# Kernel tuning notes

Measured on AMD Instinct MI355X. Metric: run time of the kernel, lower is better.

## Reference

```python
import math
import jax, jax.numpy as jnp
import numpy as np

B, NQ, NK, DIM, H, HD = 2, 1024, 2048, 1024, 16, 64


def setup_inputs() -> dict:
    key = jax.random.key(0)
    ks = jax.random.split(key, 12)
    s = 1.0 / math.sqrt(DIM)
    return {
        "q": jax.random.normal(ks[0], (B, NQ, DIM), jnp.float32),
        "k": jax.random.normal(ks[1], (B, NK, DIM), jnp.float32),
        "v": jax.random.normal(ks[2], (B, NK, DIM), jnp.float32),
        "distances": jax.random.uniform(ks[3], (B, NQ, NK), jnp.float32),
        "attn_mask": jax.random.bernoulli(ks[4], 0.5, (B, NQ, NK)),
        "key_padding_mask_q": jax.random.bernoulli(ks[5], 0.5, (B, NQ)),
        "key_padding_mask_k": jax.random.bernoulli(ks[6], 0.5, (B, NK)),
        "Wq": jax.random.normal(ks[7], (H * HD, DIM), jnp.float32) * s,
        "Wk": jax.random.normal(ks[8], (H * HD, DIM), jnp.float32) * s,
        "Wv": jax.random.normal(ks[9], (H * HD, DIM), jnp.float32) * s,
        "Wo": jax.random.normal(ks[10], (DIM, H * HD), jnp.float32) * s,
        "gate_alpha": jnp.float32(0.1),
    }


def reference(q, k, v, distances, attn_mask, key_padding_mask_q,
              key_padding_mask_k, Wq, Wk, Wv, Wo, gate_alpha):
    bsz, q_len, _ = q.shape
    k_len = k.shape[1]
    neg = jnp.finfo(q.dtype).min

    # projections -> (B, H, N, HD)
    qp = (q @ Wq.T).reshape(bsz, q_len, H, HD).transpose(0, 2, 1, 3)
    kp = (k @ Wk.T).reshape(bsz, k_len, H, HD).transpose(0, 2, 1, 3)
    vp = (v @ Wv.T).reshape(bsz, k_len, H, HD).transpose(0, 2, 1, 3)

    scores = jnp.einsum('bhqd,bhkd->bhqk', qp, kp) / math.sqrt(HD)
    scores = jnp.where(attn_mask[:, None, :, :], scores, neg)
    scores = jnp.where(key_padding_mask_k[:, None, None, :], scores, neg)

    attn = jax.nn.softmax(scores, axis=-1)  # (B,H,NQ,NK)

    # distance gating: mask, batch-mean normalize, exponential gate
    d = distances * attn_mask.astype(distances.dtype)
    d = d * key_padding_mask_k[:, None, :].astype(d.dtype)
    mean = d.sum(axis=(-1, -2)) / (q_len * k_len + 1e-6)
    mean = jnp.maximum(mean, 1e-6)[:, None, None]
    d = d / mean
    alpha = jax.nn.softplus(gate_alpha)
    gate = jnp.exp(-alpha * d)[:, None, :, :]  # (B,1,NQ,NK)

    w = attn * gate
    w = w / (w.sum(axis=-1, keepdims=True) + 1e-6)

    out = jnp.einsum('bhqk,bhkd->bhqd', w, vp)
    out = out.transpose(0, 2, 1, 3).reshape(bsz, q_len, H * HD)
    out = out * key_padding_mask_q[:, :, None].astype(out.dtype)
    return out @ Wo.T
```

## Files before the change

### kernel.cpp

```cpp
#include <hip/hip_runtime.h>
#include <hip/hip_bf16.h>
#include <cfloat>

#define B_   2
#define NQ_  1024
#define NK_  2048
#define H_   16
#define HD_  64
#define VPAD 2176
#define GPAD 2112

typedef float  floatx4 __attribute__((ext_vector_type(4)));
typedef __bf16 bf16x8  __attribute__((ext_vector_type(8)));
typedef __bf16 bf16x4  __attribute__((ext_vector_type(4)));

static __device__ __forceinline__ floatx4 mfma16(bf16x8 a, bf16x8 b, floatx4 c) {
    return __builtin_amdgcn_mfma_f32_16x16x32_bf16(a, b, c, 0, 0, 0);
}

struct CvtArgs {
    const float* src[7];
    __bf16*      dst[7];
};

__global__ __launch_bounds__(256) void cvt_kernel(CvtArgs a)
{
    size_t r = (size_t)blockIdx.x * 256 + threadIdx.x;
    int s;
    if (r < 262144)                  { s = 0; }
    else if ((r -= 262144) < 524288) { s = 1; }
    else if ((r -= 524288) < 524288) { s = 2; }
    else { r -= 524288; s = 3 + (int)(r >> 17); r &= 131071; }
    const float* sp = a.src[s] + r * 8;
    float4 f0 = *(const float4*)sp;
    float4 f1 = *(const float4*)(sp + 4);
    bf16x8 o;
    o[0] = (__bf16)f0.x; o[1] = (__bf16)f0.y; o[2] = (__bf16)f0.z; o[3] = (__bf16)f0.w;
    o[4] = (__bf16)f1.x; o[5] = (__bf16)f1.y; o[6] = (__bf16)f1.z; o[7] = (__bf16)f1.w;
    *(bf16x8*)(a.dst[s] + r * 8) = o;
}

__global__ __launch_bounds__(256) void mean_kernel(
    const float* __restrict__ dist, const int* __restrict__ amask,
    const int* __restrict__ kpmk, float* __restrict__ msum)
{
    const int b = blockIdx.y;
    const float* d  = dist  + (size_t)b * NQ_ * NK_;
    const int*   am = amask + (size_t)b * NQ_ * NK_;
    const int*   km = kpmk  + b * NK_;
    const int total = NQ_ * NK_ / 4;
    float s = 0.f;
    for (int i = blockIdx.x * blockDim.x + threadIdx.x; i < total;
         i += gridDim.x * blockDim.x) {
        const int idx = i * 4;
        const int kk  = idx & (NK_ - 1);
        float4 dv = *(const float4*)(d + idx);
        int4   mv = *(const int4*)(am + idx);
        int4   kv = *(const int4*)(km + kk);
        s += (mv.x && kv.x) ? dv.x : 0.f;
        s += (mv.y && kv.y) ? dv.y : 0.f;
        s += (mv.z && kv.z) ? dv.z : 0.f;
        s += (mv.w && kv.w) ? dv.w : 0.f;
    }
    #pragma unroll
    for (int off = 32; off >= 1; off >>= 1) s += __shfl_down(s, off);
    __shared__ float wsum[4];
    if ((threadIdx.x & 63) == 0) wsum[threadIdx.x >> 6] = s;
    __syncthreads();
    if (threadIdx.x == 0)
        atomicAdd(&msum[b], wsum[0] + wsum[1] + wsum[2] + wsum[3]);
}

__global__ __launch_bounds__(256) void gate_kernel(
    const float* __restrict__ dist, const int* __restrict__ amask,
    const int* __restrict__ kpmk, const float* __restrict__ msum,
    const float* __restrict__ galpha, __bf16* __restrict__ gate)
{
    const int b = blockIdx.y;
    const float mean  = fmaxf(msum[b] / ((float)(NQ_ * NK_) + 1e-6f), 1e-6f);
    const float alpha = log1pf(__expf(galpha[0]));
    const float c     = -alpha / mean;
    const int i  = blockIdx.x * 256 + threadIdx.x;
    const int q  = i >> 9;
    const int k4 = (i & 511) * 4;
    const size_t src = ((size_t)b * NQ_ + q) * NK_ + k4;
    float4 dv = *(const float4*)(dist + src);
    int4   mv = *(const int4*)(amask + src);
    int4   kv = *(const int4*)(kpmk + b * NK_ + k4);
    bf16x4 r;
    r[0] = (mv.x && kv.x) ? (__bf16)__expf(c * dv.x) : (__bf16)0.f;
    r[1] = (mv.y && kv.y) ? (__bf16)__expf(c * dv.y) : (__bf16)0.f;
    r[2] = (mv.z && kv.z) ? (__bf16)__expf(c * dv.z) : (__bf16)0.f;
    r[3] = (mv.w && kv.w) ? (__bf16)__expf(c * dv.w) : (__bf16)0.f;
    *(bf16x4*)&gate[((size_t)b * NQ_ + q) * GPAD + k4] = r;
}

template <int MODE>
__global__ __launch_bounds__(256) void gemm64(
    const __bf16* __restrict__ A, const __bf16* __restrict__ Bw,
    void* __restrict__ Cout)
{
    __shared__ __bf16 As[4 * 64 * 8];
    __shared__ __bf16 Bs[4 * 128 * 8];
    const int t    = threadIdx.x;
    const int m0   = blockIdx.x * 64, n0 = blockIdx.y * 128;
    const int w    = t >> 6, lane = t & 63;
    const int lrow = lane & 15, quad = lane >> 4;

    const int rowA = t >> 2, cA = t & 3;
    const int rowB1 = 64 + (t >> 2);
    const __bf16* Ag  = A  + (size_t)(m0 + rowA) * 1024 + cA * 8;
    const __bf16* Bg0 = Bw + (size_t)(n0 + rowA) * 1024 + cA * 8;
    const __bf16* Bg1 = Bw + (size_t)(n0 + rowB1) * 1024 + cA * 8;
    __bf16* AsW  = &As[cA * 512  + rowA * 8];
    __bf16* BsW0 = &Bs[cA * 1024 + rowA * 8];
    __bf16* BsW1 = &Bs[cA * 1024 + rowB1 * 8];

    floatx4 acc[4][2];
    #pragma unroll
    for (int mi = 0; mi < 4; mi++)
        #pragma unroll
        for (int ni = 0; ni < 2; ni++) acc[mi][ni] = floatx4{0.f, 0.f, 0.f, 0.f};

    bf16x8 ar  = *(const bf16x8*)Ag;
    bf16x8 br0 = *(const bf16x8*)Bg0;
    bf16x8 br1 = *(const bf16x8*)Bg1;

    for (int k0 = 0; k0 < 1024; k0 += 32) {
        __syncthreads();
        *(bf16x8*)AsW  = ar;
        *(bf16x8*)BsW0 = br0;
        *(bf16x8*)BsW1 = br1;
        __syncthreads();
        if (k0 + 32 < 1024) {
            ar  = *(const bf16x8*)(Ag  + k0 + 32);
            br0 = *(const bf16x8*)(Bg0 + k0 + 32);
            br1 = *(const bf16x8*)(Bg1 + k0 + 32);
        }
        bf16x8 af[4], bfr[2];
        #pragma unroll
        for (int mi = 0; mi < 4; mi++)
            af[mi] = *(const bf16x8*)&As[quad * 512 + (mi * 16 + lrow) * 8];
        #pragma unroll
        for (int ni = 0; ni < 2; ni++)
            bfr[ni] = *(const bf16x8*)&Bs[quad * 1024 + (w * 32 + ni * 16 + lrow) * 8];
        #pragma unroll
        for (int mi = 0; mi < 4; mi++)
            #pragma unroll
            for (int ni = 0; ni < 2; ni++)
                acc[mi][ni] = mfma16(af[mi], bfr[ni], acc[mi][ni]);
    }

    #pragma unroll
    for (int mi = 0; mi < 4; mi++) {
        #pragma unroll
        for (int ni = 0; ni < 2; ni++) {
            #pragma unroll
            for (int r = 0; r < 4; r++) {
                const float val = acc[mi][ni][r];
                const int m = m0 + mi * 16 + quad * 4 + r;
                const int n = n0 + w * 32 + ni * 16 + lrow;
                if constexpr (MODE == 0) {
                    const int b = m >> 10, q = m & 1023;
                    const int h = n >> 6,  d = n & 63;
                    ((__bf16*)Cout)[(((size_t)(b * 16 + h) * NQ_ + q) << 6) + d] =
                        (__bf16)val;
                } else if constexpr (MODE == 1) {
                    const int b = m >> 11, key = m & 2047;
                    const int h = n >> 6,  d = n & 63;
                    ((__bf16*)Cout)[(((size_t)(b * 16 + h) * NK_ + key) << 6) + d] =
                        (__bf16)val;
                } else if constexpr (MODE == 2) {
                    const int b = m >> 11, key = m & 2047;
                    const int h = n >> 6,  d = n & 63;
                    ((__bf16*)Cout)[((size_t)(b * 16 + h) * HD_ + d) * VPAD + key] =
                        (__bf16)val;
                } else {
                    ((float*)Cout)[(size_t)m * 1024 + n] = val;
                }
            }
        }
    }
}

__global__ __launch_bounds__(256, 2) void attn_kernel(
    const __bf16* __restrict__ qp, const __bf16* __restrict__ kp,
    const __bf16* __restrict__ vpT, const __bf16* __restrict__ gate,
    float* __restrict__ Opart, float* __restrict__ Gpart)
{
    __shared__ __bf16 Ks[64 * 72];
    __shared__ __bf16 Vt[64 * 72];
    __shared__ __bf16 Ps[4][32 * 72];
    const int t    = threadIdx.x;
    const int w    = t >> 6, lane = t & 63;
    const int lrow = lane & 15, quad = lane >> 4;
    const int qt   = blockIdx.x;
    const int bh   = blockIdx.y;
    const int sp   = blockIdx.z;
    const int b    = bh >> 4;
    const int q0   = qt * 128 + w * 32;
    const int k0   = sp * (NK_ / 2);

    bf16x8 qf[2][2];
    #pragma unroll
    for (int qg = 0; qg < 2; qg++) {
        const __bf16* qb = qp + ((size_t)bh * NQ_ + q0 + qg * 16 + lrow) * HD_ +
                           quad * 8;
        qf[qg][0] = *(const bf16x8*)qb;
        qf[qg][1] = *(const bf16x8*)(qb + 32);
    }

    const int srow0 = t >> 3,        sc0 = t & 7;
    const int srow1 = 32 + (t >> 3), sc1 = t & 7;
    const __bf16* Kg = kp  + (size_t)bh * NK_ * HD_;
    const __bf16* Vg = vpT + (size_t)bh * HD_ * VPAD;
    __bf16* KsW0 = &Ks[srow0 * 72 + sc0 * 8];
    __bf16* KsW1 = &Ks[srow1 * 72 + sc1 * 8];
    __bf16* VtW0 = &Vt[srow0 * 72 + sc0 * 8];
    __bf16* VtW1 = &Vt[srow1 * 72 + sc1 * 8];

    const __bf16* grow[2];
    #pragma unroll
    for (int qg = 0; qg < 2; qg++)
        grow[qg] = gate + ((size_t)b * NQ_ + q0 + qg * 16 + lrow) * GPAD;

    float G[2] = {0.f, 0.f};
    floatx4 O[2][4];
    #pragma unroll
    for (int qg = 0; qg < 2; qg++)
        #pragma unroll
        for (int nb = 0; nb < 4; nb++) O[qg][nb] = floatx4{0.f, 0.f, 0.f, 0.f};

    bf16x8 kr0, kr1, vr0, vr1;
    bf16x4 gr[2][4];
    auto loadt = [&](int kb) {
        kr0 = *(const bf16x8*)(Kg + (size_t)(kb + srow0) * HD_ + sc0 * 8);
        kr1 = *(const bf16x8*)(Kg + (size_t)(kb + srow1) * HD_ + sc1 * 8);
        vr0 = *(const bf16x8*)(Vg + (size_t)srow0 * VPAD + kb + sc0 * 8);
        vr1 = *(const bf16x8*)(Vg + (size_t)srow1 * VPAD + kb + sc1 * 8);
        #pragma unroll
        for (int qg = 0; qg < 2; qg++)
            #pragma unroll
            for (int c = 0; c < 4; c++)
                gr[qg][c] = *(const bf16x4*)(grow[qg] + kb + c * 16 + quad * 4);
    };
    loadt(k0);

    for (int kb = k0; kb < k0 + NK_ / 2; kb += 64) {
        __syncthreads();
        *(bf16x8*)KsW0 = kr0;
        *(bf16x8*)KsW1 = kr1;
        *(bf16x8*)VtW0 = vr0;
        *(bf16x8*)VtW1 = vr1;
        __syncthreads();

        bf16x4 gcur[2][4];
        #pragma unroll
        for (int qg = 0; qg < 2; qg++)
            #pragma unroll
            for (int c = 0; c < 4; c++) gcur[qg][c] = gr[qg][c];
        if (kb + 64 < k0 + NK_ / 2) loadt(kb + 64);

        bf16x8 kf0[4], kf1[4];
        #pragma unroll
        for (int c = 0; c < 4; c++) {
            kf0[c] = *(const bf16x8*)&Ks[(c * 16 + lrow) * 72 + quad * 8];
            kf1[c] = *(const bf16x8*)&Ks[(c * 16 + lrow) * 72 + 32 + quad * 8];
        }
        floatx4 s4[2][4];
        #pragma unroll
        for (int qg = 0; qg < 2; qg++)
            #pragma unroll
            for (int c = 0; c < 4; c++) {
                floatx4 a = floatx4{0.f, 0.f, 0.f, 0.f};
                a = mfma16(kf0[c], qf[qg][0], a);
                a = mfma16(kf1[c], qf[qg][1], a);
                s4[qg][c] = a;
            }

        #pragma unroll
        for (int qg = 0; qg < 2; qg++) {
            #pragma unroll
            for (int c = 0; c < 4; c++) {
                const float e0 = __expf(s4[qg][c][0] * 0.125f) * (float)gcur[qg][c][0];
                const float e1 = __expf(s4[qg][c][1] * 0.125f) * (float)gcur[qg][c][1];
                const float e2 = __expf(s4[qg][c][2] * 0.125f) * (float)gcur[qg][c][2];
                const float e3 = __expf(s4[qg][c][3] * 0.125f) * (float)gcur[qg][c][3];
                G[qg] += (e0 + e1) + (e2 + e3);
                bf16x4 pk;
                pk[0] = (__bf16)e0; pk[1] = (__bf16)e1;
                pk[2] = (__bf16)e2; pk[3] = (__bf16)e3;
                *(bf16x4*)&Ps[w][(qg * 16 + lrow) * 72 + c * 16 + quad * 4] = pk;
            }
        }

        bf16x8 pf[2][2];
        #pragma unroll
        for (int qg = 0; qg < 2; qg++)
            #pragma unroll
            for (int tt = 0; tt < 2; tt++)
                pf[qg][tt] = *(const bf16x8*)
                    &Ps[w][(qg * 16 + lrow) * 72 + tt * 32 + quad * 8];
        #pragma unroll
        for (int tt = 0; tt < 2; tt++)
            #pragma unroll
            for (int nb = 0; nb < 4; nb++) {
                bf16x8 vf = *(const bf16x8*)
                    &Vt[(nb * 16 + lrow) * 72 + tt * 32 + quad * 8];
                #pragma unroll
                for (int qg = 0; qg < 2; qg++)
                    O[qg][nb] = mfma16(pf[qg][tt], vf, O[qg][nb]);
            }
    }

    #pragma unroll
    for (int qg = 0; qg < 2; qg++) {
        G[qg] += __shfl_xor(G[qg], 16);
        G[qg] += __shfl_xor(G[qg], 32);
    }
    float* Ob = Opart + ((size_t)(sp * 32 + bh) * NQ_ + q0) * HD_;
    #pragma unroll
    for (int qg = 0; qg < 2; qg++)
        #pragma unroll
        for (int nb = 0; nb < 4; nb++)
            #pragma unroll
            for (int r = 0; r < 4; r++)
                Ob[(size_t)(qg * 16 + quad * 4 + r) * HD_ + nb * 16 + lrow] =
                    O[qg][nb][r];
    if (quad == 0) {
        #pragma unroll
        for (int qg = 0; qg < 2; qg++)
            Gpart[(size_t)(sp * 32 + bh) * NQ_ + q0 + qg * 16 + lrow] = G[qg];
    }
}

__global__ __launch_bounds__(256) void combine_kernel(
    const float* __restrict__ Opart, const float* __restrict__ Gpart,
    const int* __restrict__ kpmq, __bf16* __restrict__ attnout)
{
    const int t  = blockIdx.x * 256 + threadIdx.x;
    const int d4 = (t & 15) * 4;
    const int q  = (t >> 4) & 1023;
    const int bh = t >> 14;
    const int b  = bh >> 4, h = bh & 15;
    const size_t i0 = ((size_t)bh * NQ_ + q) * HD_ + d4;
    const size_t i1 = ((size_t)(32 + bh) * NQ_ + q) * HD_ + d4;
    float4 o0 = *(const float4*)(Opart + i0);
    float4 o1 = *(const float4*)(Opart + i1);
    const float g = Gpart[bh * NQ_ + q] + Gpart[(32 + bh) * NQ_ + q];
    const float f = kpmq[b * NQ_ + q] ? 1.f / (g + 1e-30f) : 0.f;
    bf16x4 r;
    r[0] = (__bf16)((o0.x + o1.x) * f);
    r[1] = (__bf16)((o0.y + o1.y) * f);
    r[2] = (__bf16)((o0.z + o1.z) * f);
    r[3] = (__bf16)((o0.w + o1.w) * f);
    *(bf16x4*)&attnout[((size_t)b * NQ_ + q) * 1024 + h * HD_ + d4] = r;
}

extern "C" void kernel_launch(void* const* d_in, const int* in_sizes, int n_in,
                              void* d_out, int out_size, void* d_ws,
                              size_t ws_size, hipStream_t stream)
{
    const float* q      = (const float*)d_in[0];
    const float* k      = (const float*)d_in[1];
    const float* v      = (const float*)d_in[2];
    const float* dist   = (const float*)d_in[3];
    const int*   amask  = (const int*)d_in[4];
    const int*   kpmq   = (const int*)d_in[5];
    const int*   kpmk   = (const int*)d_in[6];
    const float* Wq     = (const float*)d_in[7];
    const float* Wk     = (const float*)d_in[8];
    const float* Wv     = (const float*)d_in[9];
    const float* Wo     = (const float*)d_in[10];
    const float* galpha = (const float*)d_in[11];

    char* p = (char*)d_ws;
    float*  msum = (float*)p;                 p += 256;
    __bf16* qb   = (__bf16*)p;                p += (size_t)2097152 * 2;
    __bf16* kb   = (__bf16*)p;                p += (size_t)4194304 * 2;
    __bf16* vb   = (__bf16*)p;                p += (size_t)4194304 * 2;
    __bf16* wqb  = (__bf16*)p;                p += (size_t)1048576 * 2;
    __bf16* wkb  = (__bf16*)p;                p += (size_t)1048576 * 2;
    __bf16* wvb  = (__bf16*)p;                p += (size_t)1048576 * 2;
    __bf16* wob  = (__bf16*)p;                p += (size_t)1048576 * 2;
    __bf16* qp   = (__bf16*)p;                p += (size_t)2097152 * 2;
    __bf16* kpb  = (__bf16*)p;                p += (size_t)4194304 * 2;
    __bf16* vpT  = (__bf16*)p;                p += (size_t)32 * 64 * VPAD * 2;
    __bf16* gate = (__bf16*)p;                p += (size_t)2048 * GPAD * 2;
    __bf16* attnout = (__bf16*)p;             p += (size_t)2097152 * 2;
    float*  Opart   = (float*)p;              p += (size_t)2 * 2097152 * 4;
    float*  Gpart   = (float*)p;              p += (size_t)65536 * 4;

    CvtArgs ca;
    ca.src[0] = q;  ca.src[1] = k;  ca.src[2] = v;
    ca.src[3] = Wq; ca.src[4] = Wk; ca.src[5] = Wv; ca.src[6] = Wo;
    ca.dst[0] = qb;  ca.dst[1] = kb;  ca.dst[2] = vb;
    ca.dst[3] = wqb; ca.dst[4] = wkb; ca.dst[5] = wvb; ca.dst[6] = wob;

    hipMemsetAsync(msum, 0, 256, stream);
    cvt_kernel<<<7168, 256, 0, stream>>>(ca);
    mean_kernel<<<dim3(128, 2), 256, 0, stream>>>(dist, amask, kpmk, msum);
    gate_kernel<<<dim3(2048, 2), 256, 0, stream>>>(dist, amask, kpmk, msum,
                                                   galpha, gate);
    gemm64<0><<<dim3(32, 8), 256, 0, stream>>>(qb, wqb, qp);
    gemm64<1><<<dim3(64, 8), 256, 0, stream>>>(kb, wkb, kpb);
    gemm64<2><<<dim3(64, 8), 256, 0, stream>>>(vb, wvb, vpT);
    attn_kernel<<<dim3(8, 32, 2), 256, 0, stream>>>(qp, kpb, vpT, gate,
                                                    Opart, Gpart);
    combine_kernel<<<2048, 256, 0, stream>>>(Opart, Gpart, kpmq, attnout);
    gemm64<3><<<dim3(32, 8), 256, 0, stream>>>(attnout, wob, (float*)d_out);
}
```

Measured before the change: 275.6 us.

## Use 128x128 GEMM tiles with direct global-to-LDS loads, fuse QKV projections, split keys four ways

Replaces the 64x128 register-staged GEMM with a 128x128 tile core that copies global memory straight into LDS through the global_load_lds builtin. The Q, K and V projections now run as one merged launch, and the output projection uses the same core. The attention key dimension is split four ways instead of two, with launch bounds raised to 4 waves per SIMD, so more blocks can run in parallel. The trade-offs are the loss of prefetch overlap in the GEMM, which now has two barriers and no double buffering, and more partial-sum memory and traffic in the combine step.

```diff
diff --git a/kernel.cpp b/kernel.cpp
--- a/kernel.cpp
+++ b/kernel.cpp
@@ -9,6 +9,7 @@
 #define HD_  64
 #define VPAD 2176
 #define GPAD 2112
+#define NSPLIT 4
 
 typedef float  floatx4 __attribute__((ext_vector_type(4)));
 typedef __bf16 bf16x8  __attribute__((ext_vector_type(8)));
@@ -16,6 +17,17 @@
 
 static __device__ __forceinline__ floatx4 mfma16(bf16x8 a, bf16x8 b, floatx4 c) {
     return __builtin_amdgcn_mfma_f32_16x16x32_bf16(a, b, c, 0, 0, 0);
+}
+
+static __device__ __forceinline__ void gl_lds(const __bf16* g, __bf16* lbase,
+                                              int lane) {
+#if __has_builtin(__builtin_amdgcn_global_load_lds)
+    __builtin_amdgcn_global_load_lds(
+        (const __attribute__((address_space(1))) void*)g,
+        (__attribute__((address_space(3))) void*)lbase, 16, 0, 0);
+#else
+    *(bf16x8*)(lbase + lane * 8) = *(const bf16x8*)g;
+#endif
 }
 
 struct CvtArgs {
@@ -95,95 +107,114 @@
     *(bf16x4*)&gate[((size_t)b * NQ_ + q) * GPAD + k4] = r;
 }
 
-template <int MODE>
-__global__ __launch_bounds__(256) void gemm64(
+template <typename EPI>
+static __device__ __forceinline__ void gemm128_core(
     const __bf16* __restrict__ A, const __bf16* __restrict__ Bw,
-    void* __restrict__ Cout)
-{
-    __shared__ __bf16 As[4 * 64 * 8];
-    __shared__ __bf16 Bs[4 * 128 * 8];
+    int m0, int n0, EPI epi)
+{
+    __shared__ alignas(16) __bf16 As[128 * 32];
+    __shared__ alignas(16) __bf16 Bs[128 * 32];
     const int t    = threadIdx.x;
-    const int m0   = blockIdx.x * 64, n0 = blockIdx.y * 128;
     const int w    = t >> 6, lane = t & 63;
     const int lrow = lane & 15, quad = lane >> 4;
-
-    const int rowA = t >> 2, cA = t & 3;
-    const int rowB1 = 64 + (t >> 2);
-    const __bf16* Ag  = A  + (size_t)(m0 + rowA) * 1024 + cA * 8;
-    const __bf16* Bg0 = Bw + (size_t)(n0 + rowA) * 1024 + cA * 8;
-    const __bf16* Bg1 = Bw + (size_t)(n0 + rowB1) * 1024 + cA * 8;
-    __bf16* AsW  = &As[cA * 512  + rowA * 8];
-    __bf16* BsW0 = &Bs[cA * 1024 + rowA * 8];
-    __bf16* BsW1 = &Bs[cA * 1024 + rowB1 * 8];
-
-    floatx4 acc[4][2];
+    const int lr   = lane >> 2, lc = lane & 3;
+
+    floatx4 acc[4][4];
     #pragma unroll
     for (int mi = 0; mi < 4; mi++)
         #pragma unroll
-        for (int ni = 0; ni < 2; ni++) acc[mi][ni] = floatx4{0.f, 0.f, 0.f, 0.f};
-
-    bf16x8 ar  = *(const bf16x8*)Ag;
-    bf16x8 br0 = *(const bf16x8*)Bg0;
-    bf16x8 br1 = *(const bf16x8*)Bg1;
+        for (int ni = 0; ni < 4; ni++) acc[mi][ni] = floatx4{0.f, 0.f, 0.f, 0.f};
+
+    const __bf16* ga = A  + (size_t)(m0 + w * 32 + lr) * 1024 + lc * 8;
+    const __bf16* gb = Bw + (size_t)(n0 + w * 32 + lr) * 1024 + lc * 8;
+    __bf16* la0 = &As[(w * 32) * 32];
+    __bf16* la1 = &As[(w * 32 + 16) * 32];
+    __bf16* lb0 = &Bs[(w * 32) * 32];
+    __bf16* lb1 = &Bs[(w * 32 + 16) * 32];
 
     for (int k0 = 0; k0 < 1024; k0 += 32) {
         __syncthreads();
-        *(bf16x8*)AsW  = ar;
-        *(bf16x8*)BsW0 = br0;
-        *(bf16x8*)BsW1 = br1;
+        gl_lds(ga + k0,              la0, lane);
+        gl_lds(ga + k0 + 16 * 1024,  la1, lane);
+        gl_lds(gb + k0,              lb0, lane);
+        gl_lds(gb + k0 + 16 * 1024,  lb1, lane);
         __syncthreads();
-        if (k0 + 32 < 1024) {
-            ar  = *(const bf16x8*)(Ag  + k0 + 32);
-            br0 = *(const bf16x8*)(Bg0 + k0 + 32);
-            br1 = *(const bf16x8*)(Bg1 + k0 + 32);
-        }
-        bf16x8 af[4], bfr[2];
+
+        bf16x8 af[4], bfr[4];
         #pragma unroll
         for (int mi = 0; mi < 4; mi++)
-            af[mi] = *(const bf16x8*)&As[quad * 512 + (mi * 16 + lrow) * 8];
-        #pragma unroll
-        for (int ni = 0; ni < 2; ni++)
-            bfr[ni] = *(const bf16x8*)&Bs[quad * 1024 + (w * 32 + ni * 16 + lrow) * 8];
+            af[mi] = *(const bf16x8*)
+                &As[((w & 1) * 64 + mi * 16 + lrow) * 32 + quad * 8];
+        #pragma unroll
+        for (int ni = 0; ni < 4; ni++)
+            bfr[ni] = *(const bf16x8*)
+                &Bs[((w >> 1) * 64 + ni * 16 + lrow) * 32 + quad * 8];
         #pragma unroll
         for (int mi = 0; mi < 4; mi++)
             #pragma unroll
-            for (int ni = 0; ni < 2; ni++)
+            for (int ni = 0; ni < 4; ni++)
                 acc[mi][ni] = mfma16(af[mi], bfr[ni], acc[mi][ni]);
     }
 
     #pragma unroll
-    for (int mi = 0; mi < 4; mi++) {
-        #pragma unroll
-        for (int ni = 0; ni < 2; ni++) {
+    for (int mi = 0; mi < 4; mi++)
+        #pragma unroll
+        for (int ni = 0; ni < 4; ni++)
             #pragma unroll
             for (int r = 0; r < 4; r++) {
-                const float val = acc[mi][ni][r];
-                const int m = m0 + mi * 16 + quad * 4 + r;
-                const int n = n0 + w * 32 + ni * 16 + lrow;
-                if constexpr (MODE == 0) {
-                    const int b = m >> 10, q = m & 1023;
-                    const int h = n >> 6,  d = n & 63;
-                    ((__bf16*)Cout)[(((size_t)(b * 16 + h) * NQ_ + q) << 6) + d] =
-                        (__bf16)val;
-                } else if constexpr (MODE == 1) {
-                    const int b = m >> 11, key = m & 2047;
-                    const int h = n >> 6,  d = n & 63;
-                    ((__bf16*)Cout)[(((size_t)(b * 16 + h) * NK_ + key) << 6) + d] =
-                        (__bf16)val;
-                } else if constexpr (MODE == 2) {
-                    const int b = m >> 11, key = m & 2047;
-                    const int h = n >> 6,  d = n & 63;
-                    ((__bf16*)Cout)[((size_t)(b * 16 + h) * HD_ + d) * VPAD + key] =
-                        (__bf16)val;
-                } else {
-                    ((float*)Cout)[(size_t)m * 1024 + n] = val;
-                }
+                const int m = m0 + (w & 1) * 64 + mi * 16 + quad * 4 + r;
+                const int n = n0 + (w >> 1) * 64 + ni * 16 + lrow;
+                epi(m, n, acc[mi][ni][r]);
             }
-        }
-    }
-}
-
-__global__ __launch_bounds__(256, 2) void attn_kernel(
+}
+
+__global__ __launch_bounds__(256) void proj_kernel(
+    const __bf16* __restrict__ qb, const __bf16* __restrict__ kb,
+    const __bf16* __restrict__ vb, const __bf16* __restrict__ wqb,
+    const __bf16* __restrict__ wkb, const __bf16* __restrict__ wvb,
+    __bf16* __restrict__ qp, __bf16* __restrict__ kp,
+    __bf16* __restrict__ vpT)
+{
+    const int z = blockIdx.z;
+    const __bf16* A; const __bf16* W; int mtiles;
+    if (z == 0)      { A = qb; W = wqb; mtiles = 16; }
+    else if (z == 1) { A = kb; W = wkb; mtiles = 32; }
+    else             { A = vb; W = wvb; mtiles = 32; }
+    if ((int)blockIdx.x >= mtiles) return;
+    const int m0 = blockIdx.x * 128, n0 = blockIdx.y * 128;
+
+    if (z == 0) {
+        gemm128_core(A, W, m0, n0, [&](int m, int n, float v) {
+            const int b = m >> 10, q = m & 1023;
+            const int h = n >> 6,  d = n & 63;
+            qp[(((size_t)(b * 16 + h) * NQ_ + q) << 6) + d] = (__bf16)v;
+        });
+    } else if (z == 1) {
+        gemm128_core(A, W, m0, n0, [&](int m, int n, float v) {
+            const int b = m >> 11, key = m & 2047;
+            const int h = n >> 6,  d = n & 63;
+            kp[(((size_t)(b * 16 + h) * NK_ + key) << 6) + d] = (__bf16)v;
+        });
+    } else {
+        gemm128_core(A, W, m0, n0, [&](int m, int n, float v) {
+            const int b = m >> 11, key = m & 2047;
+            const int h = n >> 6,  d = n & 63;
+            vpT[((size_t)(b * 16 + h) * HD_ + d) * VPAD + key] = (__bf16)v;
+        });
+    }
+}
+
+__global__ __launch_bounds__(256) void oproj_kernel(
+    const __bf16* __restrict__ A, const __bf16* __restrict__ W,
+    float* __restrict__ Cout)
+{
+    const int m0 = blockIdx.x * 128, n0 = blockIdx.y * 128;
+    gemm128_core(A, W, m0, n0, [&](int m, int n, float v) {
+        Cout[(size_t)m * 1024 + n] = v;
+    });
+}
+
+__global__ __launch_bounds__(256, 4) void attn_kernel(
     const __bf16* __restrict__ qp, const __bf16* __restrict__ kp,
     const __bf16* __restrict__ vpT, const __bf16* __restrict__ gate,
     float* __restrict__ Opart, float* __restrict__ Gpart)
@@ -199,7 +230,7 @@
     const int sp   = blockIdx.z;
     const int b    = bh >> 4;
     const int q0   = qt * 128 + w * 32;
-    const int k0   = sp * (NK_ / 2);
+    const int k0   = sp * (NK_ / NSPLIT);
 
     bf16x8 qf[2][2];
     #pragma unroll
@@ -246,7 +277,7 @@
     };
     loadt(k0);
 
-    for (int kb = k0; kb < k0 + NK_ / 2; kb += 64) {
+    for (int kb = k0; kb < k0 + NK_ / NSPLIT; kb += 64) {
         __syncthreads();
         *(bf16x8*)KsW0 = kr0;
         *(bf16x8*)KsW1 = kr1;
@@ -259,7 +290,7 @@
         for (int qg = 0; qg < 2; qg++)
             #pragma unroll
             for (int c = 0; c < 4; c++) gcur[qg][c] = gr[qg][c];
-        if (kb + 64 < k0 + NK_ / 2) loadt(kb + 64);
+        if (kb + 64 < k0 + NK_ / NSPLIT) loadt(kb + 64);
 
         bf16x8 kf0[4], kf1[4];
         #pragma unroll
@@ -343,17 +374,21 @@
     const int q  = (t >> 4) & 1023;
     const int bh = t >> 14;
     const int b  = bh >> 4, h = bh & 15;
-    const size_t i0 = ((size_t)bh * NQ_ + q) * HD_ + d4;
-    const size_t i1 = ((size_t)(32 + bh) * NQ_ + q) * HD_ + d4;
-    float4 o0 = *(const float4*)(Opart + i0);
-    float4 o1 = *(const float4*)(Opart + i1);
-    const float g = Gpart[bh * NQ_ + q] + Gpart[(32 + bh) * NQ_ + q];
+    float4 o = float4{0.f, 0.f, 0.f, 0.f};
+    float  g = 0.f;
+    #pragma unroll
+    for (int j = 0; j < NSPLIT; j++) {
+        float4 oj = *(const float4*)
+            (Opart + ((size_t)(j * 32 + bh) * NQ_ + q) * HD_ + d4);
+        o.x += oj.x; o.y += oj.y; o.z += oj.z; o.w += oj.w;
+        g += Gpart[(size_t)(j * 32 + bh) * NQ_ + q];
+    }
     const float f = kpmq[b * NQ_ + q] ? 1.f / (g + 1e-30f) : 0.f;
     bf16x4 r;
-    r[0] = (__bf16)((o0.x + o1.x) * f);
-    r[1] = (__bf16)((o0.y + o1.y) * f);
-    r[2] = (__bf16)((o0.z + o1.z) * f);
-    r[3] = (__bf16)((o0.w + o1.w) * f);
+    r[0] = (__bf16)(o.x * f);
+    r[1] = (__bf16)(o.y * f);
+    r[2] = (__bf16)(o.z * f);
+    r[3] = (__bf16)(o.w * f);
     *(bf16x4*)&attnout[((size_t)b * NQ_ + q) * 1024 + h * HD_ + d4] = r;
 }
 
@@ -388,8 +423,8 @@
     __bf16* vpT  = (__bf16*)p;                p += (size_t)32 * 64 * VPAD * 2;
     __bf16* gate = (__bf16*)p;                p += (size_t)2048 * GPAD * 2;
     __bf16* attnout = (__bf16*)p;             p += (size_t)2097152 * 2;
-    float*  Opart   = (float*)p;              p += (size_t)2 * 2097152 * 4;
-    float*  Gpart   = (float*)p;              p += (size_t)65536 * 4;
+    float*  Opart   = (float*)p;              p += (size_t)NSPLIT * 2097152 * 4;
+    float*  Gpart   = (float*)p;              p += (size_t)NSPLIT * 32768 * 4;
 
     CvtArgs ca;
     ca.src[0] = q;  ca.src[1] = k;  ca.src[2] = v;
@@ -402,11 +437,10 @@
     mean_kernel<<<dim3(128, 2), 256, 0, stream>>>(dist, amask, kpmk, msum);
     gate_kernel<<<dim3(2048, 2), 256, 0, stream>>>(dist, amask, kpmk, msum,
                                                    galpha, gate);
-    gemm64<0><<<dim3(32, 8), 256, 0, stream>>>(qb, wqb, qp);
-    gemm64<1><<<dim3(64, 8), 256, 0, stream>>>(kb, wkb, kpb);
-    gemm64<2><<<dim3(64, 8), 256, 0, stream>>>(vb, wvb, vpT);
-    attn_kernel<<<dim3(8, 32, 2), 256, 0, stream>>>(qp, kpb, vpT, gate,
-                                                    Opart, Gpart);
+    proj_kernel<<<dim3(32, 8, 3), 256, 0, stream>>>(qb, kb, vb, wqb, wkb, wvb,
+                                                    qp, kpb, vpT);
+    attn_kernel<<<dim3(8, 32, NSPLIT), 256, 0, stream>>>(qp, kpb, vpT, gate,
+                                                         Opart, Gpart);
     combine_kernel<<<2048, 256, 0, stream>>>(Opart, Gpart, kpmq, attnout);
-    gemm64<3><<<dim3(32, 8), 256, 0, stream>>>(attnout, wob, (float*)d_out);
-}
+    oproj_kernel<<<dim3(16, 8), 256, 0, stream>>>(attnout, wob, (float*)d_out);
+}
```

Measured after the change: 324.3 us. +17.7%, slower.
